# Performance work log

Measured on AMD Instinct MI355X. Metric: run time of the kernel, lower is better.

Reference implementation:

```python
import jax, jax.numpy as jnp
import numpy as np

ALPHA = 0.2          # LeakyReLU negative slope
NEG_INF = -9e15      # mask value used by the torch module


def setup_inputs() -> dict:
    key = jax.random.key(0)
    k_x, k_adj, k_w, k_a = jax.random.split(key, 4)
    B, N, D, L = 8, 2048, 128, 3
    x = jax.random.normal(k_x, (B, N, D), dtype=jnp.float32)
    adj = jax.random.randint(k_adj, (B, N, N), 0, 2, dtype=jnp.int32)
    Wg = jax.random.normal(k_w, (L, D, D), dtype=jnp.float32) * 0.08  # ~Linear init scale
    bg = jnp.zeros((L, D), dtype=jnp.float32)
    attn_a = jax.random.normal(k_a, (L, 2 * D), dtype=jnp.float32) * 0.08
    return {"x": x, "adj": adj, "Wg": Wg, "bg": bg, "attn_a": attn_a}


def reference(x, adj, Wg, bg, attn_a):
    # x: [B,N,D], adj: [B,N,N] int, Wg: [L,D,D], bg: [L,D], attn_a: [L,2D]
    D = x.shape[-1]
    L = Wg.shape[0]
    mask = adj > 0
    for i in range(L):  # small fixed layer loop
        h = jax.nn.relu(x @ Wg[i] + bg[i])                       # [B,N,D]
        # a_input[b,i,j] = [h_i, h_j]; dot with a splits into two rank-1 terms,
        # avoiding the N*N*2D intermediate while computing identical math.
        s1 = h @ attn_a[i, :D]                                   # [B,N]
        s2 = h @ attn_a[i, D:]                                   # [B,N]
        e = jax.nn.leaky_relu(s1[:, :, None] + s2[:, None, :], ALPHA)  # [B,N,N]
        e = jnp.where(mask, e, NEG_INF)
        attn = jax.nn.softmax(e, axis=2)                         # masked softmax over neighbors
        # dropout p=0.0 -> identity
        x = x + jnp.einsum('bij,bjd->bid', attn, h)              # residual update
    return x
```

## Files before the change

### kernel.cpp

```cpp
#include <hip/hip_runtime.h>
#include <stdint.h>

typedef __attribute__((ext_vector_type(8))) short short8;
typedef __attribute__((ext_vector_type(4))) float f32x4;
typedef __attribute__((ext_vector_type(16))) float f32x16;
typedef __attribute__((ext_vector_type(4))) unsigned uint4v;

__device__ __forceinline__ unsigned short f2bf(float f) {
    unsigned u = __float_as_uint(f);
    unsigned r = u + 0x7fffu + ((u >> 16) & 1u);
    return (unsigned short)(r >> 16);
}
__device__ __forceinline__ unsigned fenc(float f) {
    unsigned u = __float_as_uint(f);
    return (u & 0x80000000u) ? ~u : (u | 0x80000000u);
}
__device__ __forceinline__ float fdec(unsigned e) {
    unsigned u = (e & 0x80000000u) ? (e & 0x7fffffffu) : ~e;
    return __uint_as_float(u);
}

__global__ __launch_bounds__(256) void k_setup(
    const float* __restrict__ xin, const float* __restrict__ Wf,
    const int* __restrict__ adj, float* __restrict__ xq,
    unsigned short* __restrict__ wTb, unsigned* __restrict__ s2mx,
    unsigned long long* __restrict__ packed)
{
    int blk = blockIdx.x, tid = threadIdx.x;
    if (blk < 2048) {
        int w = (blk * 256 + tid) >> 6;
        int lane = tid & 63;
        for (int k = 0; k < 64; k++) {
            int q = w * 64 + k;
            int row = q >> 5, wd = q & 31;
            int v = adj[row * 2048 + wd * 64 + lane];
            unsigned long long m = __ballot(v > 0);
            if (lane == 0) packed[q] = m;
        }
    } else if (blk < 4096) {
        int e0 = ((blk - 2048) * 256 + tid) * 4;
        *(f32x4*)(xq + e0) = *(const f32x4*)(xin + e0);
    } else if (blk < 4288) {
        int c = (blk - 4096) * 256 + tid;
        int l = c >> 14, rem = c & 16383, n = rem >> 7, k = rem & 127;
        wTb[c] = f2bf(Wf[l * 16384 + k * 128 + n]);
    } else if (tid < 24) {
        s2mx[tid] = fenc(-3e38f);
    }
}

__global__ __launch_bounds__(256) void k_h(
    const float* __restrict__ xq, const unsigned short* __restrict__ wTb,
    const float* __restrict__ bF, const float* __restrict__ aF, int layer,
    unsigned short* __restrict__ hP, float* __restrict__ s1g,
    float* __restrict__ s2g, unsigned* __restrict__ s2mx)
{
    __shared__ short xs[64 * 136];
    __shared__ short wsb[128 * 136];
    __shared__ float s2blk[4];
    int blk = blockIdx.x, tid = threadIdx.x;
    int row0 = blk * 64, b = blk >> 5;
    int w = tid >> 6, lane = tid & 63, quad = lane >> 4, l15 = lane & 15;

    for (int c = tid; c < 1024; c += 256) {
        int r = c >> 4, kg = c & 15;
        const float* src = &xq[(row0 + r) * 128 + kg * 8];
        f32x4 v0 = *(const f32x4*)src;
        f32x4 v1 = *(const f32x4*)(src + 4);
        short8 o;
        o[0] = (short)f2bf(v0[0]); o[1] = (short)f2bf(v0[1]);
        o[2] = (short)f2bf(v0[2]); o[3] = (short)f2bf(v0[3]);
        o[4] = (short)f2bf(v1[0]); o[5] = (short)f2bf(v1[1]);
        o[6] = (short)f2bf(v1[2]); o[7] = (short)f2bf(v1[3]);
        *(short8*)&xs[r * 136 + kg * 8] = o;
    }
    const unsigned short* wl = wTb + layer * 16384;
    for (int c = tid; c < 2048; c += 256) {
        int n = c >> 4, kg = c & 15;
        *(short8*)&wsb[n * 136 + kg * 8] = *(const short8*)&wl[n * 128 + kg * 8];
    }
    __syncthreads();

    f32x4 acc[8];
#pragma unroll
    for (int t = 0; t < 8; t++) acc[t] = {0.f, 0.f, 0.f, 0.f};
#pragma unroll
    for (int ks = 0; ks < 4; ks++) {
        short8 af = *(const short8*)&xs[(w * 16 + l15) * 136 + ks * 32 + quad * 8];
#pragma unroll
        for (int t = 0; t < 8; t++) {
            short8 bf = *(const short8*)&wsb[(t * 16 + l15) * 136 + ks * 32 + quad * 8];
            acc[t] = __builtin_amdgcn_mfma_f32_16x16x32_bf16(af, bf, acc[t], 0, 0, 0);
        }
    }

    float s1p[4] = {0.f, 0.f, 0.f, 0.f}, s2p[4] = {0.f, 0.f, 0.f, 0.f};
#pragma unroll
    for (int t = 0; t < 8; t++) {
        int colg = t * 16 + l15;
        float bgf = bF[layer * 128 + colg];
        float a1 = aF[layer * 256 + colg];
        float a2 = aF[layer * 256 + 128 + colg];
#pragma unroll
        for (int r = 0; r < 4; r++) {
            float v = acc[t][r] + bgf;
            v = v > 0.f ? v : 0.f;
            acc[t][r] = v;
            s1p[r] = fmaf(v, a1, s1p[r]);
            s2p[r] = fmaf(v, a2, s2p[r]);
        }
    }
#pragma unroll
    for (int r = 0; r < 4; r++) {
#pragma unroll
        for (int off = 1; off < 16; off <<= 1) {
            s1p[r] += __shfl_xor(s1p[r], off, 64);
            s2p[r] += __shfl_xor(s2p[r], off, 64);
        }
    }
    if (l15 == 0) {
#pragma unroll
        for (int r = 0; r < 4; r++) {
            int rowg = row0 + w * 16 + quad * 4 + r;
            s1g[rowg] = s1p[r];
            s2g[rowg] = s2p[r];
        }
    }
    float mx = fmaxf(fmaxf(s2p[0], s2p[1]), fmaxf(s2p[2], s2p[3]));
    mx = fmaxf(mx, __shfl_xor(mx, 16, 64));
    mx = fmaxf(mx, __shfl_xor(mx, 32, 64));
    if (lane == 0) s2blk[w] = mx;
    __syncthreads();

    short* st = (short*)wsb;
#pragma unroll
    for (int t = 0; t < 8; t++)
#pragma unroll
        for (int r = 0; r < 4; r++)
            st[(w * 16 + quad * 4 + r) * 130 + t * 16 + l15] = (short)f2bf(acc[t][r]);
    __syncthreads();
    if (tid == 0) {
        float m2 = fmaxf(fmaxf(s2blk[0], s2blk[1]), fmaxf(s2blk[2], s2blk[3]));
        atomicMax(&s2mx[layer * 8 + b], fenc(m2));
    }
    int i0 = (blk & 31) * 64;
    for (int c = tid; c < 1024; c += 256) {
        int t = c >> 8, jl2 = (c >> 6) & 3, sl = c & 63;
        int d = t * 32 + (sl & 31);
        int jloc = jl2 * 16 + (sl >> 5) * 8;
        short8 o;
#pragma unroll
        for (int i = 0; i < 8; i++) o[i] = st[(jloc + i) * 130 + d];
        int jtg = (i0 >> 4) + jl2;
        *(short8*)&hP[(((size_t)(b * 4 + t) * 128 + jtg) * 64 + sl) * 8] = o;
    }
}

__global__ __launch_bounds__(256) void k_attn(
    const unsigned long long* __restrict__ packed,
    const unsigned short* __restrict__ hP, const float* __restrict__ s1g,
    const float* __restrict__ s2g, const unsigned* __restrict__ s2mx,
    int layer, float* __restrict__ xq)
{
    __shared__ float red[3 * 32 * 128];
    __shared__ float red_p[4 * 32];
    int blk = blockIdx.x, tid = threadIdx.x;
    int b = blk >> 6;
    int rowg0 = blk * 32;
    int w = tid >> 6, lane = tid & 63;
    int col = lane & 31, khalf = lane >> 5;

    float s1v = s1g[rowg0 + col];
    float s2m = fdec(s2mx[layer * 8 + b]);
    float tmh = s1v + s2m;
    float mhat = fmaxf(tmh, 0.2f * tmh);

    f32x16 acc[5];
#pragma unroll
    for (int t = 0; t < 5; t++)
#pragma unroll
        for (int r = 0; r < 16; r++) acc[t][r] = 0.f;

    short8 onesf;
    {
        short v = (col == 0) ? (short)0x3F80 : (short)0;
        onesf[0]=v;onesf[1]=v;onesf[2]=v;onesf[3]=v;onesf[4]=v;onesf[5]=v;onesf[6]=v;onesf[7]=v;
    }

    const float* s2b = s2g + b * 2048;
    const unsigned short* hPb = hP + (size_t)b * 4 * 128 * 64 * 8;
    const unsigned long long* prow = packed + (size_t)(rowg0 + col) * 32;

    for (int jl = 0; jl < 32; jl++) {
        int jt = w + jl * 4;
        unsigned long long word = prow[jl];
        unsigned b8 = (unsigned)(word >> (w * 16 + khalf * 8)) & 0xffu;
        int j0 = jt * 16 + khalf * 8;
        f32x4 sa = *(const f32x4*)&s2b[j0];
        f32x4 sb = *(const f32x4*)&s2b[j0 + 4];
        float sv[8] = {sa[0], sa[1], sa[2], sa[3], sb[0], sb[1], sb[2], sb[3]};
        unsigned rp[8];
#pragma unroll
        for (int jj = 0; jj < 8; jj++) {
            float e = s1v + sv[jj];
            e = fmaxf(e, 0.2f * e);
            float pv = __expf(e - mhat);
            rp[jj] = (b8 & (1u << jj)) ? (__float_as_uint(pv) + 0x8000u) : 0u;
        }
        uint4v pk;
        pk[0] = (rp[0] >> 16) | (rp[1] & 0xffff0000u);
        pk[1] = (rp[2] >> 16) | (rp[3] & 0xffff0000u);
        pk[2] = (rp[4] >> 16) | (rp[5] & 0xffff0000u);
        pk[3] = (rp[6] >> 16) | (rp[7] & 0xffff0000u);
        short8 af = *(short8*)&pk;
        short8 bfr[4];
#pragma unroll
        for (int t = 0; t < 4; t++)
            bfr[t] = *(const short8*)&hPb[(((size_t)t * 128 + jt) * 64 + lane) * 8];
#pragma unroll
        for (int t = 0; t < 4; t++)
            acc[t] = __builtin_amdgcn_mfma_f32_32x32x16_bf16(af, bfr[t], acc[t], 0, 0, 0);
        acc[4] = __builtin_amdgcn_mfma_f32_32x32x16_bf16(af, onesf, acc[4], 0, 0, 0);
    }

#pragma unroll
    for (int reg = 0; reg < 16; reg++) {
        int row = (reg & 3) + 8 * (reg >> 2) + 4 * khalf;
        if (w > 0) {
#pragma unroll
            for (int t = 0; t < 4; t++)
                red[(w - 1) * 4096 + row * 128 + t * 32 + col] = acc[t][reg];
        }
        if (col == 0) red_p[w * 32 + row] = acc[4][reg];
    }
    __syncthreads();
    if (w == 0) {
#pragma unroll
        for (int reg = 0; reg < 16; reg++) {
            int row = (reg & 3) + 8 * (reg >> 2) + 4 * khalf;
            float p = red_p[row] + red_p[32 + row] + red_p[64 + row] + red_p[96 + row];
            float rl = p > 0.f ? 1.0f / p : 0.f;
#pragma unroll
            for (int t = 0; t < 4; t++) {
                int cidx = row * 128 + t * 32 + col;
                float o = acc[t][reg] + red[cidx] + red[4096 + cidx] + red[8192 + cidx];
                xq[(rowg0 + row) * 128 + t * 32 + col] += o * rl;
            }
        }
    }
}

extern "C" void kernel_launch(void* const* d_in, const int* in_sizes, int n_in,
                              void* d_out, int out_size, void* d_ws, size_t ws_size,
                              hipStream_t stream) {
    const void* px = d_in[0];
    int ia = 1; long amax = -1;
    for (int i = 1; i < n_in; i++)
        if ((long)in_sizes[i] > amax) { amax = in_sizes[i]; ia = i; }
    int rem[8]; int m = 0;
    for (int i = 1; i < n_in && m < 8; i++) if (i != ia) rem[m++] = i;
    for (int i = 0; i < m; i++)
        for (int j = i + 1; j < m; j++)
            if (in_sizes[rem[j]] > in_sizes[rem[i]]) { int t = rem[i]; rem[i] = rem[j]; rem[j] = t; }
    const int*   padj = (const int*)((n_in > 1) ? d_in[ia] : d_in[0]);
    const float* pW = (const float*)((m > 0) ? d_in[rem[0]] : d_in[0]);
    const float* pa = (const float*)((m > 1) ? d_in[rem[1]] : d_in[0]);
    const float* pb = (const float*)((m > 2) ? d_in[rem[2]] : d_in[0]);

    float* xq = (float*)d_out;
    char* ws = (char*)d_ws;
    unsigned long long* packed = (unsigned long long*)ws;
    unsigned short* hP = (unsigned short*)(ws + 4194304);
    float* s1 = (float*)(ws + 8388608);
    float* s2 = (float*)(ws + 8454144);
    unsigned* s2mx = (unsigned*)(ws + 8519680);
    unsigned short* wTb = (unsigned short*)(ws + 8519808);

    k_setup<<<4289, 256, 0, stream>>>((const float*)px, pW, padj, xq, wTb, s2mx, packed);
    for (int l = 0; l < 3; l++) {
        k_h<<<256, 256, 0, stream>>>(xq, wTb, pb, pa, l, hP, s1, s2, s2mx);
        k_attn<<<512, 256, 0, stream>>>(packed, hP, s1, s2, s2mx, l, xq);
    }
}
```

Before: 344.8 us.

## Restructure attention kernel to share P tiles via LDS and split D across waves

k_attn now has each wave compute the masked exp probabilities for its own j-slice and publish them to shared memory. Every wave then multiplies all four P slices against its own 32-column slice of h, so the cross-wave reduction of full accumulators is removed. The loads for the next step are double-buffered, the masking uses a LUT with packed bf16 conversion, and exp2 is applied with log2e folded into the attention vector. k_h switches to 512 threads with column-split waves and interleaved batch block order. This adds a __syncthreads per j-step and more LDS traffic in exchange for fewer accumulator registers and no final reduction.

```diff
diff --git a/kernel.cpp b/kernel.cpp
--- a/kernel.cpp
+++ b/kernel.cpp
@@ -6,6 +6,8 @@
 typedef __attribute__((ext_vector_type(16))) float f32x16;
 typedef __attribute__((ext_vector_type(4))) unsigned uint4v;
 
+#define LOG2E 1.4426950408889634f
+
 __device__ __forceinline__ unsigned short f2bf(float f) {
     unsigned u = __float_as_uint(f);
     unsigned r = u + 0x7fffu + ((u >> 16) & 1u);
@@ -18,6 +20,11 @@
 __device__ __forceinline__ float fdec(unsigned e) {
     unsigned u = (e & 0x80000000u) ? (e & 0x7fffffffu) : ~e;
     return __uint_as_float(u);
+}
+__device__ __forceinline__ unsigned cvt_pk_bf16(float lo, float hi) {
+    unsigned r;
+    asm("v_cvt_pk_bf16_f32 %0, %1, %2" : "=v"(r) : "v"(lo), "v"(hi));
+    return r;
 }
 
 __global__ __launch_bounds__(256) void k_setup(
@@ -49,7 +56,7 @@
     }
 }
 
-__global__ __launch_bounds__(256) void k_h(
+__global__ __launch_bounds__(512) void k_h(
     const float* __restrict__ xq, const unsigned short* __restrict__ wTb,
     const float* __restrict__ bF, const float* __restrict__ aF, int layer,
     unsigned short* __restrict__ hP, float* __restrict__ s1g,
@@ -57,12 +64,14 @@
 {
     __shared__ short xs[64 * 136];
     __shared__ short wsb[128 * 136];
-    __shared__ float s2blk[4];
+    __shared__ float s12[2][2][64];
     int blk = blockIdx.x, tid = threadIdx.x;
-    int row0 = blk * 64, b = blk >> 5;
-    int w = tid >> 6, lane = tid & 63, quad = lane >> 4, l15 = lane & 15;
-
-    for (int c = tid; c < 1024; c += 256) {
+    int b = blk & 7, rg = blk >> 3;
+    int row0 = b * 2048 + rg * 64;
+    int lane = tid & 63, quad = lane >> 4, l15 = lane & 15;
+    int wv = tid >> 6, rw = wv & 3, ch = wv >> 2;
+
+    for (int c = tid; c < 1024; c += 512) {
         int r = c >> 4, kg = c & 15;
         const float* src = &xq[(row0 + r) * 128 + kg * 8];
         f32x4 v0 = *(const f32x4*)src;
@@ -75,32 +84,32 @@
         *(short8*)&xs[r * 136 + kg * 8] = o;
     }
     const unsigned short* wl = wTb + layer * 16384;
-    for (int c = tid; c < 2048; c += 256) {
+    for (int c = tid; c < 2048; c += 512) {
         int n = c >> 4, kg = c & 15;
         *(short8*)&wsb[n * 136 + kg * 8] = *(const short8*)&wl[n * 128 + kg * 8];
     }
     __syncthreads();
 
-    f32x4 acc[8];
-#pragma unroll
-    for (int t = 0; t < 8; t++) acc[t] = {0.f, 0.f, 0.f, 0.f};
+    f32x4 acc[4];
+#pragma unroll
+    for (int t = 0; t < 4; t++) acc[t] = {0.f, 0.f, 0.f, 0.f};
 #pragma unroll
     for (int ks = 0; ks < 4; ks++) {
-        short8 af = *(const short8*)&xs[(w * 16 + l15) * 136 + ks * 32 + quad * 8];
-#pragma unroll
-        for (int t = 0; t < 8; t++) {
-            short8 bf = *(const short8*)&wsb[(t * 16 + l15) * 136 + ks * 32 + quad * 8];
+        short8 af = *(const short8*)&xs[(rw * 16 + l15) * 136 + ks * 32 + quad * 8];
+#pragma unroll
+        for (int t = 0; t < 4; t++) {
+            short8 bf = *(const short8*)&wsb[((ch * 4 + t) * 16 + l15) * 136 + ks * 32 + quad * 8];
             acc[t] = __builtin_amdgcn_mfma_f32_16x16x32_bf16(af, bf, acc[t], 0, 0, 0);
         }
     }
 
     float s1p[4] = {0.f, 0.f, 0.f, 0.f}, s2p[4] = {0.f, 0.f, 0.f, 0.f};
 #pragma unroll
-    for (int t = 0; t < 8; t++) {
-        int colg = t * 16 + l15;
+    for (int t = 0; t < 4; t++) {
+        int colg = (ch * 4 + t) * 16 + l15;
         float bgf = bF[layer * 128 + colg];
-        float a1 = aF[layer * 256 + colg];
-        float a2 = aF[layer * 256 + 128 + colg];
+        float a1 = aF[layer * 256 + colg] * LOG2E;
+        float a2 = aF[layer * 256 + 128 + colg] * LOG2E;
 #pragma unroll
         for (int r = 0; r < 4; r++) {
             float v = acc[t][r] + bgf;
@@ -121,40 +130,79 @@
     if (l15 == 0) {
 #pragma unroll
         for (int r = 0; r < 4; r++) {
-            int rowg = row0 + w * 16 + quad * 4 + r;
-            s1g[rowg] = s1p[r];
-            s2g[rowg] = s2p[r];
-        }
-    }
-    float mx = fmaxf(fmaxf(s2p[0], s2p[1]), fmaxf(s2p[2], s2p[3]));
-    mx = fmaxf(mx, __shfl_xor(mx, 16, 64));
-    mx = fmaxf(mx, __shfl_xor(mx, 32, 64));
-    if (lane == 0) s2blk[w] = mx;
+            int rloc = rw * 16 + quad * 4 + r;
+            s12[0][ch][rloc] = s1p[r];
+            s12[1][ch][rloc] = s2p[r];
+        }
+    }
     __syncthreads();
 
     short* st = (short*)wsb;
 #pragma unroll
-    for (int t = 0; t < 8; t++)
+    for (int t = 0; t < 4; t++)
 #pragma unroll
         for (int r = 0; r < 4; r++)
-            st[(w * 16 + quad * 4 + r) * 130 + t * 16 + l15] = (short)f2bf(acc[t][r]);
-    __syncthreads();
-    if (tid == 0) {
-        float m2 = fmaxf(fmaxf(s2blk[0], s2blk[1]), fmaxf(s2blk[2], s2blk[3]));
-        atomicMax(&s2mx[layer * 8 + b], fenc(m2));
-    }
-    int i0 = (blk & 31) * 64;
-    for (int c = tid; c < 1024; c += 256) {
+            st[(rw * 16 + quad * 4 + r) * 130 + (ch * 4 + t) * 16 + l15] = (short)f2bf(acc[t][r]);
+
+    if (tid < 64) {
+        float s1 = s12[0][0][tid] + s12[0][1][tid];
+        float s2 = s12[1][0][tid] + s12[1][1][tid];
+        s1g[row0 + tid] = s1;
+        s2g[row0 + tid] = s2;
+        float mx = s2;
+#pragma unroll
+        for (int off = 1; off < 64; off <<= 1)
+            mx = fmaxf(mx, __shfl_xor(mx, off, 64));
+        if (tid == 0) atomicMax(&s2mx[layer * 8 + b], fenc(mx));
+    }
+    __syncthreads();
+    int jt0 = rg * 4;
+    for (int c = tid; c < 1024; c += 512) {
         int t = c >> 8, jl2 = (c >> 6) & 3, sl = c & 63;
         int d = t * 32 + (sl & 31);
         int jloc = jl2 * 16 + (sl >> 5) * 8;
         short8 o;
 #pragma unroll
         for (int i = 0; i < 8; i++) o[i] = st[(jloc + i) * 130 + d];
-        int jtg = (i0 >> 4) + jl2;
-        *(short8*)&hP[(((size_t)(b * 4 + t) * 128 + jtg) * 64 + sl) * 8] = o;
-    }
-}
+        *(short8*)&hP[(((size_t)(b * 4 + t) * 128 + (jt0 + jl2)) * 64 + sl) * 8] = o;
+    }
+}
+
+#define GAT_STEP(JL, CUR, NXT)                                                  \
+  {                                                                             \
+    unsigned b8 = (unsigned)(wdv[CUR] >> joff) & 0xffu;                         \
+    float pv[8];                                                                \
+    _Pragma("unroll")                                                           \
+    for (int jj = 0; jj < 4; jj++) {                                            \
+      float v0 = s1fold + sA[CUR][jj];                                          \
+      float v1 = s1fold + sB[CUR][jj];                                          \
+      pv[jj]     = __builtin_amdgcn_exp2f(fmaxf(v0, fmaf(0.2f, v0, c8)));       \
+      pv[jj + 4] = __builtin_amdgcn_exp2f(fmaxf(v1, fmaf(0.2f, v1, c8)));       \
+    }                                                                           \
+    uint4v pk;                                                                  \
+    pk[0] = cvt_pk_bf16(pv[0], pv[1]) & lutq[0][b8];                            \
+    pk[1] = cvt_pk_bf16(pv[2], pv[3]) & lutq[1][b8];                            \
+    pk[2] = cvt_pk_bf16(pv[4], pv[5]) & lutq[2][b8];                            \
+    pk[3] = cvt_pk_bf16(pv[6], pv[7]) & lutq[3][b8];                            \
+    short8 af = *(short8*)&pk;                                                  \
+    *(short8*)&pshare[CUR][w][lane * 8] = af;                                   \
+    ps = __builtin_amdgcn_mfma_f32_32x32x16_bf16(af, onesf, ps, 0, 0, 0);       \
+    if ((JL) + 1 < 32) {                                                        \
+      wdv[NXT] = prow[(JL) + 1];                                                \
+      int j0n = ((JL) + 1) * 64 + joff;                                         \
+      sA[NXT] = *(const f32x4*)&s2gb[j0n];                                      \
+      sB[NXT] = *(const f32x4*)&s2gb[j0n + 4];                                  \
+      _Pragma("unroll")                                                         \
+      for (int q = 0; q < 4; q++)                                               \
+        bfr[NXT][q] = *(const short8*)&hPb[((size_t)(w * 128 + ((JL) + 1) * 4 + q) * 64 + lane) * 8]; \
+    }                                                                           \
+    __syncthreads();                                                            \
+    _Pragma("unroll")                                                           \
+    for (int q = 0; q < 4; q++) {                                               \
+      short8 pf = *(short8*)&pshare[CUR][q][lane * 8];                          \
+      acc = __builtin_amdgcn_mfma_f32_32x32x16_bf16(pf, bfr[CUR][q], acc, 0, 0, 0); \
+    }                                                                           \
+  }
 
 __global__ __launch_bounds__(256) void k_attn(
     const unsigned long long* __restrict__ packed,
@@ -162,24 +210,29 @@
     const float* __restrict__ s2g, const unsigned* __restrict__ s2mx,
     int layer, float* __restrict__ xq)
 {
-    __shared__ float red[3 * 32 * 128];
-    __shared__ float red_p[4 * 32];
+    __shared__ unsigned lutq[4][256];
+    __shared__ short pshare[2][4][512];
+    __shared__ float red_p[4][32];
     int blk = blockIdx.x, tid = threadIdx.x;
-    int b = blk >> 6;
-    int rowg0 = blk * 32;
+    int b = blk & 7, rg = blk >> 3;
+    int rowg0 = b * 2048 + rg * 32;
     int w = tid >> 6, lane = tid & 63;
     int col = lane & 31, khalf = lane >> 5;
+
+    {
+        unsigned e = (unsigned)tid;
+#pragma unroll
+        for (int q = 0; q < 4; q++)
+            lutq[q][e] = (((e >> (2 * q)) & 1u) ? 0xffffu : 0u) |
+                         (((e >> (2 * q + 1)) & 1u) ? 0xffff0000u : 0u);
+    }
 
     float s1v = s1g[rowg0 + col];
     float s2m = fdec(s2mx[layer * 8 + b]);
     float tmh = s1v + s2m;
     float mhat = fmaxf(tmh, 0.2f * tmh);
-
-    f32x16 acc[5];
-#pragma unroll
-    for (int t = 0; t < 5; t++)
-#pragma unroll
-        for (int r = 0; r < 16; r++) acc[t][r] = 0.f;
+    float s1fold = s1v - mhat;
+    float c8 = -0.8f * mhat;
 
     short8 onesf;
     {
@@ -187,66 +240,45 @@
         onesf[0]=v;onesf[1]=v;onesf[2]=v;onesf[3]=v;onesf[4]=v;onesf[5]=v;onesf[6]=v;onesf[7]=v;
     }
 
-    const float* s2b = s2g + b * 2048;
+    const float* s2gb = s2g + b * 2048;
     const unsigned short* hPb = hP + (size_t)b * 4 * 128 * 64 * 8;
     const unsigned long long* prow = packed + (size_t)(rowg0 + col) * 32;
-
-    for (int jl = 0; jl < 32; jl++) {
-        int jt = w + jl * 4;
-        unsigned long long word = prow[jl];
-        unsigned b8 = (unsigned)(word >> (w * 16 + khalf * 8)) & 0xffu;
-        int j0 = jt * 16 + khalf * 8;
-        f32x4 sa = *(const f32x4*)&s2b[j0];
-        f32x4 sb = *(const f32x4*)&s2b[j0 + 4];
-        float sv[8] = {sa[0], sa[1], sa[2], sa[3], sb[0], sb[1], sb[2], sb[3]};
-        unsigned rp[8];
-#pragma unroll
-        for (int jj = 0; jj < 8; jj++) {
-            float e = s1v + sv[jj];
-            e = fmaxf(e, 0.2f * e);
-            float pv = __expf(e - mhat);
-            rp[jj] = (b8 & (1u << jj)) ? (__float_as_uint(pv) + 0x8000u) : 0u;
-        }
-        uint4v pk;
-        pk[0] = (rp[0] >> 16) | (rp[1] & 0xffff0000u);
-        pk[1] = (rp[2] >> 16) | (rp[3] & 0xffff0000u);
-        pk[2] = (rp[4] >> 16) | (rp[5] & 0xffff0000u);
-        pk[3] = (rp[6] >> 16) | (rp[7] & 0xffff0000u);
-        short8 af = *(short8*)&pk;
-        short8 bfr[4];
-#pragma unroll
-        for (int t = 0; t < 4; t++)
-            bfr[t] = *(const short8*)&hPb[(((size_t)t * 128 + jt) * 64 + lane) * 8];
-#pragma unroll
-        for (int t = 0; t < 4; t++)
-            acc[t] = __builtin_amdgcn_mfma_f32_32x32x16_bf16(af, bfr[t], acc[t], 0, 0, 0);
-        acc[4] = __builtin_amdgcn_mfma_f32_32x32x16_bf16(af, onesf, acc[4], 0, 0, 0);
+    int joff = w * 16 + khalf * 8;
+
+    f32x16 acc, ps;
+#pragma unroll
+    for (int r = 0; r < 16; r++) { acc[r] = 0.f; ps[r] = 0.f; }
+
+    unsigned long long wdv[2];
+    f32x4 sA[2], sB[2];
+    short8 bfr[2][4];
+
+    wdv[0] = prow[0];
+    sA[0] = *(const f32x4*)&s2gb[joff];
+    sB[0] = *(const f32x4*)&s2gb[joff + 4];
+#pragma unroll
+    for (int q = 0; q < 4; q++)
+        bfr[0][q] = *(const short8*)&hPb[((size_t)(w * 128 + q) * 64 + lane) * 8];
+    __syncthreads();
+
+#pragma unroll 1
+    for (int jl = 0; jl < 32; jl += 2) {
+        GAT_STEP(jl, 0, 1)
+        GAT_STEP(jl + 1, 1, 0)
     }
 
 #pragma unroll
     for (int reg = 0; reg < 16; reg++) {
         int row = (reg & 3) + 8 * (reg >> 2) + 4 * khalf;
-        if (w > 0) {
-#pragma unroll
-            for (int t = 0; t < 4; t++)
-                red[(w - 1) * 4096 + row * 128 + t * 32 + col] = acc[t][reg];
-        }
-        if (col == 0) red_p[w * 32 + row] = acc[4][reg];
-    }
-    __syncthreads();
-    if (w == 0) {
-#pragma unroll
-        for (int reg = 0; reg < 16; reg++) {
-            int row = (reg & 3) + 8 * (reg >> 2) + 4 * khalf;
-            float p = red_p[row] + red_p[32 + row] + red_p[64 + row] + red_p[96 + row];
-            float rl = p > 0.f ? 1.0f / p : 0.f;
-#pragma unroll
-            for (int t = 0; t < 4; t++) {
-                int cidx = row * 128 + t * 32 + col;
-                float o = acc[t][reg] + red[cidx] + red[4096 + cidx] + red[8192 + cidx];
-                xq[(rowg0 + row) * 128 + t * 32 + col] += o * rl;
-            }
-        }
+        if (col == 0) red_p[w][row] = ps[reg];
+    }
+    __syncthreads();
+#pragma unroll
+    for (int reg = 0; reg < 16; reg++) {
+        int row = (reg & 3) + 8 * (reg >> 2) + 4 * khalf;
+        float p = red_p[0][row] + red_p[1][row] + red_p[2][row] + red_p[3][row];
+        float rl = p > 0.f ? __builtin_amdgcn_rcpf(p) : 0.f;
+        xq[(rowg0 + row) * 128 + w * 32 + col] += acc[reg] * rl;
     }
 }
 
@@ -278,7 +310,7 @@
 
     k_setup<<<4289, 256, 0, stream>>>((const float*)px, pW, padj, xq, wTb, s2mx, packed);
     for (int l = 0; l < 3; l++) {
-        k_h<<<256, 256, 0, stream>>>(xq, wTb, pb, pa, l, hP, s1, s2, s2mx);
+        k_h<<<256, 512, 0, stream>>>(xq, wTb, pb, pa, l, hP, s1, s2, s2mx);
         k_attn<<<512, 256, 0, stream>>>(packed, hP, s1, s2, s2mx, l, xq);
     }
 }
```

Result: faster. 315.1 us (median of 2 runs) (-8.6%).
